# Kernel optimization log

Measured on AMD Instinct MI355X. Metric: run time of the kernel, lower is better.

The kernel has to match this reference:

```python
import jax, jax.numpy as jnp
import numpy as np

ROPE_BASE = 10000.0
NUM_HEADS = 16

def _rotate_half(x):
    d = x.shape[-1] // 2
    return jnp.concatenate([-x[..., d:], x[..., :d]], axis=-1)

def setup_inputs() -> dict:
    key = jax.random.key(0)
    ks = jax.random.split(key, 5)
    b, s, d = 1, 2048, 2048
    scale = 1.0 / np.sqrt(d)
    return {
        "hidden_states": jax.random.normal(ks[0], (b, s, d), jnp.float32),
        "wq": jax.random.normal(ks[1], (d, d), jnp.float32) * scale,
        "wk": jax.random.normal(ks[2], (d, d), jnp.float32) * scale,
        "wv": jax.random.normal(ks[3], (d, d), jnp.float32) * scale,
        "wo": jax.random.normal(ks[4], (d, d), jnp.float32) * scale,
        "position_ids": jnp.broadcast_to(jnp.arange(s, dtype=jnp.int32), (b, s)),
    }

def reference(hidden_states, wq, wk, wv, wo, position_ids):
    b, s, d = hidden_states.shape
    h = NUM_HEADS
    dh = d // h
    # q/k/v projections (torch Linear: y = x @ W^T), split heads -> bhsd
    def proj(w):
        return jnp.einsum('bsd,ed->bse', hidden_states, w).reshape(b, s, h, dh).transpose(0, 2, 1, 3)
    q, k, v = proj(wq), proj(wk), proj(wv)
    # rotary embedding (LLaMA style): freqs over half dim, duplicated
    inv_freq = 1.0 / (ROPE_BASE ** (jnp.arange(0, dh, 2, dtype=jnp.float32) / dh))
    t = jnp.arange(s, dtype=jnp.float32)
    freqs = jnp.einsum('s,f->sf', t, inv_freq)              # [s, dh/2]
    emb = jnp.concatenate([freqs, freqs], axis=-1)          # [s, dh]
    cos = jnp.cos(emb)[position_ids][:, None, :, :]         # [b,1,s,dh]
    sin = jnp.sin(emb)[position_ids][:, None, :, :]
    q = q * cos + _rotate_half(q) * sin
    k = k * cos + _rotate_half(k) * sin
    # full (non-causal) scaled dot-product attention, as in the SDPA fast path
    scores = jnp.einsum('bhqd,bhkd->bhqk', q, k) / jnp.sqrt(jnp.float32(dh))
    attn = jax.nn.softmax(scores, axis=-1)
    out = jnp.einsum('bhqk,bhkd->bhqd', attn, v)            # [b,h,s,dh]
    out = out.transpose(0, 2, 1, 3).reshape(b, s, d)
    return jnp.einsum('bsd,ed->bse', out, wo)
```

## Files before the change

kernel.cpp:

```cpp
#include <hip/hip_runtime.h>

typedef unsigned short ushort_t;
typedef unsigned int uint32;
typedef __attribute__((ext_vector_type(8))) short short8;
typedef __attribute__((ext_vector_type(4))) float f32x4;
typedef __attribute__((ext_vector_type(2))) uint32 u32x2;

#define LDS_LOAD16(gptr, lptr)                                                             \
  __builtin_amdgcn_global_load_lds((const __attribute__((address_space(1))) uint32*)(gptr),\
                                   (__attribute__((address_space(3))) uint32*)(lptr),      \
                                   16, 0, 0)

__device__ __forceinline__ ushort_t f2b(float f) {
  uint32 u = __builtin_bit_cast(uint32, f);
  u += 0x7fffu + ((u >> 16) & 1u);
  return (ushort_t)(u >> 16);
}
__device__ __forceinline__ uint32 pk2(float a, float b) {
  return (uint32)f2b(a) | ((uint32)f2b(b) << 16);
}

constexpr size_t E = (size_t)2048 * 2048;

__global__ __launch_bounds__(256) void k_cvt5(const float* __restrict__ a0, const float* __restrict__ a1,
                                              const float* __restrict__ a2, const float* __restrict__ a3,
                                              const float* __restrict__ a4, ushort_t* __restrict__ out) {
  const float* srcs[5] = {a0, a1, a2, a3, a4};
  const float* s = srcs[blockIdx.y];
  size_t i = ((size_t)blockIdx.x * 256 + threadIdx.x) * 4;
  float4 v = *(const float4*)(s + i);
  ushort4 o;
  o.x = f2b(v.x); o.y = f2b(v.y); o.z = f2b(v.z); o.w = f2b(v.w);
  *(ushort4*)(out + (size_t)blockIdx.y * E + i) = o;
}

#define SWZ3(r) (((r) >> 1) & 3)

#define STG32(srcA, srcB, dA, dB, ktile)                                        \
  do {                                                                          \
    const int koff_ = (ktile) * 32;                                             \
    _Pragma("unroll") for (int j2_ = 0; j2_ < 2; ++j2_) {                       \
      int c_ = tid + 256 * j2_;                                                 \
      int r_ = c_ >> 2, p_ = c_ & 3;                                            \
      int sc_ = (p_ ^ SWZ3(r_)) * 8;                                            \
      LDS_LOAD16((srcA) + (row0 + r_) * 2048 + koff_ + sc_, &(dA)[c_ * 8]);     \
      LDS_LOAD16((srcB) + (col0 + r_) * 2048 + koff_ + sc_, &(dB)[c_ * 8]);     \
    }                                                                           \
  } while (0)

__global__ __launch_bounds__(256, 3) void k_gemm_qkv(const ushort_t* __restrict__ A,
                                                     const ushort_t* __restrict__ B0,
                                                     const ushort_t* __restrict__ B1,
                                                     const ushort_t* __restrict__ B2,
                                                     ushort_t* __restrict__ Qm,
                                                     ushort_t* __restrict__ Km,
                                                     ushort_t* __restrict__ Vt,
                                                     const int* __restrict__ pos) {
  __shared__ ushort_t As[3][128 * 32];
  __shared__ ushort_t Bs[3][128 * 32];
  const int tid = threadIdx.x;
  const int lane = tid & 63, wave = tid >> 6;
  const int quad = lane >> 4, l16 = lane & 15;
  const int wm = wave >> 1, wn = wave & 1;
  const int z = blockIdx.z;
  const ushort_t* Bp = (z == 0) ? B0 : (z == 1) ? B1 : B2;
  const size_t row0 = (size_t)blockIdx.y * 128, col0 = (size_t)blockIdx.x * 128;

  int g[4];
#pragma unroll
  for (int j = 0; j < 4; ++j) g[j] = (j & 1) + ((j >> 1) << 2) + wn * 2;

  f32x4 zero = {0.f, 0.f, 0.f, 0.f};
  f32x4 acc[4][4];
#pragma unroll
  for (int i = 0; i < 4; ++i)
#pragma unroll
    for (int j = 0; j < 4; ++j) acc[i][j] = zero;

#define QKV_FRAGS(CUR)                                                          \
    short8 a_[4], b_[4];                                                        \
    _Pragma("unroll") for (int i_ = 0; i_ < 4; ++i_) {                          \
      int ra_ = wm * 64 + i_ * 16 + l16;                                        \
      a_[i_] = *(const short8*)&As[CUR][(ra_ * 4 + (quad ^ SWZ3(ra_))) * 8];    \
    }                                                                           \
    _Pragma("unroll") for (int j_ = 0; j_ < 4; ++j_) {                          \
      int rb_ = g[j_] * 16 + l16;                                               \
      b_[j_] = *(const short8*)&Bs[CUR][(rb_ * 4 + (quad ^ SWZ3(rb_))) * 8];    \
    }                                                                           \
    _Pragma("unroll") for (int i_ = 0; i_ < 4; ++i_)                            \
      _Pragma("unroll") for (int j_ = 0; j_ < 4; ++j_)                          \
        acc[i_][j_] = __builtin_amdgcn_mfma_f32_16x16x32_bf16(a_[i_], b_[j_], acc[i_][j_], 0, 0, 0);

#define QKV_BODY(T, CUR, STG, SEN, VM)                                          \
  do {                                                                          \
    if (SEN) STG32(A, Bp, As[STG], Bs[STG], (T) + 2);                           \
    QKV_FRAGS(CUR)                                                              \
    asm volatile("s_waitcnt " VM ::: "memory");                                 \
    __builtin_amdgcn_s_barrier();                                               \
  } while (0)

  STG32(A, Bp, As[0], Bs[0], 0);
  STG32(A, Bp, As[1], Bs[1], 1);
  asm volatile("s_waitcnt vmcnt(4)" ::: "memory");
  __builtin_amdgcn_s_barrier();

  for (int tt = 0; tt < 60; tt += 3) {
    QKV_BODY(tt + 0, 0, 2, 1, "vmcnt(4)");
    QKV_BODY(tt + 1, 1, 0, 1, "vmcnt(4)");
    QKV_BODY(tt + 2, 2, 1, 1, "vmcnt(4)");
  }
  QKV_BODY(60, 0, 2, 1, "vmcnt(4)");
  QKV_BODY(61, 1, 0, 1, "vmcnt(4)");
  QKV_BODY(62, 2, 1, 0, "vmcnt(0)");
  { QKV_FRAGS(0) }

  if (z < 2) {
    ushort_t* C = z ? Km : Qm;
    const float mul = z ? 1.0f : 0.08838834764831845f;
#pragma unroll
    for (int i = 0; i < 4; ++i)
#pragma unroll
      for (int r = 0; r < 4; ++r) {
        size_t row = row0 + wm * 64 + i * 16 + quad * 4 + r;
        float pt = (float)pos[row];
        size_t rowoff = row * 2048 + col0;
#pragma unroll
        for (int j = 0; j < 2; ++j) {
          int f = g[j] * 16 + l16;
          float ang = pt * __expf(-0.14391156831212787f * (float)f);
          float sn, cs;
          __sincosf(ang, &sn, &cs);
          cs *= mul; sn *= mul;
          float q0 = acc[i][j][r], q1 = acc[i][j + 2][r];
          C[rowoff + f]      = f2b(q0 * cs - q1 * sn);
          C[rowoff + f + 64] = f2b(q1 * cs + q0 * sn);
        }
      }
  } else {
#pragma unroll
    for (int i = 0; i < 4; ++i)
#pragma unroll
      for (int j = 0; j < 4; ++j) {
        size_t col = col0 + g[j] * 16 + l16;
        size_t rowb = row0 + wm * 64 + i * 16 + quad * 4;
        ushort4 ov;
        ov.x = f2b(acc[i][j][0]); ov.y = f2b(acc[i][j][1]);
        ov.z = f2b(acc[i][j][2]); ov.w = f2b(acc[i][j][3]);
        *(ushort4*)&Vt[col * 2048 + rowb] = ov;
      }
  }
}

__global__ __launch_bounds__(512, 2) void k_attn(const ushort_t* __restrict__ Q,
                                                 const ushort_t* __restrict__ Kg,
                                                 const ushort_t* __restrict__ Vt,
                                                 ushort_t* __restrict__ O) {
  __shared__ uint32 smem[32768];
  ushort_t* Ks0 = (ushort_t*)smem;
  ushort_t* Ks1 = (ushort_t*)(smem + 8192);
  ushort_t* Vs  = (ushort_t*)(smem + 16384);
  uint32*   Pb  = smem + 24576;
  float*    Lred = (float*)(smem + 24576);
  float*    Rbuf = (float*)smem;

  const int tid = threadIdx.x;
  const int lane = tid & 63, wave = tid >> 6;
  const int quad = lane >> 4, l16 = lane & 15;
  const int qh = wave >> 1, kh = wave & 1;
  const int bid = blockIdx.x;
  const int head = ((bid & 7) << 1) + (bid >> 7);
  const int qt = (bid >> 3) & 15;

  const ushort_t* Kbase = Kg + (size_t)head * 128;
  const ushort_t* Vbase = Vt + (size_t)head * 128 * 2048;
  uint32* Pw = Pb + wave * 1024;

  f32x4 zero = {0.f, 0.f, 0.f, 0.f};
  short8 qr[2][4];
#pragma unroll
  for (int qg = 0; qg < 2; ++qg)
#pragma unroll
    for (int kk = 0; kk < 4; ++kk)
      qr[qg][kk] = *(const short8*)&Q[(size_t)(qt * 128 + qh * 32 + qg * 16 + l16) * 2048 +
                                      head * 128 + kk * 32 + quad * 8];

  f32x4 oacc[2][8];
#pragma unroll
  for (int qg = 0; qg < 2; ++qg)
#pragma unroll
    for (int ns = 0; ns < 8; ++ns) oacc[qg][ns] = zero;
  float l_acc[2] = {0.f, 0.f};

#define STAGE_K(KD, T)                                                           \
  _Pragma("unroll") for (int j_ = 0; j_ < 4; ++j_) {                             \
    int s_ = tid + 512 * j_; int r_ = s_ >> 4, c_ = s_ & 15;                     \
    LDS_LOAD16(Kbase + (size_t)((T) * 128 + r_) * 2048 + ((c_ ^ (r_ & 15)) * 8), \
               &(KD)[s_ * 8]);                                                   \
  }
#define STAGE_V(T)                                                               \
  _Pragma("unroll") for (int j_ = 0; j_ < 4; ++j_) {                             \
    int s_ = tid + 512 * j_; int r_ = s_ >> 4, c_ = s_ & 15;                     \
    LDS_LOAD16(Vbase + (size_t)r_ * 2048 + (T) * 128 + ((c_ ^ (r_ & 15)) * 8),   \
               &Vs[s_ * 8]);                                                     \
  }

#define ATTN_BODY(KCUR, KNXT, T, NOTLAST, VMW1)                                  \
  do {                                                                           \
    STAGE_V(T);                                                                  \
    if (NOTLAST) { STAGE_K(KNXT, (T) + 1); }                                     \
    _Pragma("unroll") for (int kg = 0; kg < 4; ++kg) {                           \
      short8 kf[4];                                                              \
      _Pragma("unroll") for (int kk = 0; kk < 4; ++kk)                           \
        kf[kk] = *(const short8*)&(KCUR)[((kh * 64 + kg * 16 + l16) * 16 +       \
                                          ((kk * 4 + quad) ^ l16)) * 8];         \
      _Pragma("unroll") for (int qg = 0; qg < 2; ++qg) {                         \
        f32x4 s = zero;                                                          \
        _Pragma("unroll") for (int kk = 0; kk < 4; ++kk)                         \
          s = __builtin_amdgcn_mfma_f32_16x16x32_bf16(kf[kk], qr[qg][kk], s, 0, 0, 0); \
        float p0 = __expf(s[0]), p1 = __expf(s[1]);                              \
        float p2 = __expf(s[2]), p3 = __expf(s[3]);                              \
        l_acc[qg] += (p0 + p1) + (p2 + p3);                                      \
        u32x2 wv; wv[0] = pk2(p0, p1); wv[1] = pk2(p2, p3);                      \
        *(u32x2*)&Pw[(qg * 16 + l16) * 32 +                                      \
                     (((kg * 2 + (quad >> 1)) ^ (l16 & 7)) << 2) +               \
                     ((quad & 1) << 1)] = wv;                                    \
      }                                                                          \
    }                                                                            \
    short8 pb[2][2];                                                             \
    _Pragma("unroll") for (int qg = 0; qg < 2; ++qg)                             \
      _Pragma("unroll") for (int ks = 0; ks < 2; ++ks)                           \
        pb[qg][ks] = *(const short8*)&Pw[(qg * 16 + l16) * 32 +                  \
                                         ((((ks << 2) + quad) ^ (l16 & 7)) << 2)]; \
    asm volatile("s_waitcnt " VMW1 ::: "memory");                                \
    __builtin_amdgcn_s_barrier();                                                \
    _Pragma("unroll") for (int ns = 0; ns < 8; ++ns)                             \
      _Pragma("unroll") for (int ks = 0; ks < 2; ++ks) {                         \
        const short8 vf = *(const short8*)&Vs[((ns * 16 + l16) * 16 +            \
                                               ((kh * 8 + ks * 4 + quad) ^ l16)) * 8]; \
        _Pragma("unroll") for (int qg = 0; qg < 2; ++qg)                         \
          oacc[qg][ns] = __builtin_amdgcn_mfma_f32_16x16x32_bf16(vf, pb[qg][ks], oacc[qg][ns], 0, 0, 0); \
      }                                                                          \
    asm volatile("s_waitcnt lgkmcnt(0)" ::: "memory");                           \
    asm volatile("s_waitcnt vmcnt(0)" ::: "memory");                             \
    __builtin_amdgcn_s_barrier();                                                \
  } while (0)

  STAGE_K(Ks0, 0);
  asm volatile("s_waitcnt vmcnt(0)" ::: "memory");
  __builtin_amdgcn_s_barrier();

  for (int t2 = 0; t2 < 14; t2 += 2) {
    ATTN_BODY(Ks0, Ks1, t2 + 0, 1, "vmcnt(4)");
    ATTN_BODY(Ks1, Ks0, t2 + 1, 1, "vmcnt(4)");
  }
  ATTN_BODY(Ks0, Ks1, 14, 1, "vmcnt(4)");
  ATTN_BODY(Ks1, Ks0, 15, 0, "vmcnt(0)");

#pragma unroll
  for (int qg = 0; qg < 2; ++qg) {
    float l = l_acc[qg];
    l += __shfl_xor(l, 16, 64);
    l += __shfl_xor(l, 32, 64);
    l_acc[qg] = l;
  }
  if (quad == 0) {
#pragma unroll
    for (int qg = 0; qg < 2; ++qg) Lred[wave * 32 + qg * 16 + l16] = l_acc[qg];
  }

  const int tq = (tid >> 4) & 15;
  const int td = (tid & 15) * 8;
  for (int p = 0; p < 8; ++p) {
    __builtin_amdgcn_s_barrier();
    if ((wave >> 1) == (p >> 1)) {
      const int qg = p & 1;
#pragma unroll
      for (int ns = 0; ns < 8; ++ns)
        *(f32x4*)&Rbuf[((kh * 16 + l16)) * 132 + ns * 16 + quad * 4] = oacc[qg][ns];
    }
    __builtin_amdgcn_s_barrier();
    if (tid < 256) {
      float lt = Lred[((p >> 1) * 2 + 0) * 32 + (p & 1) * 16 + tq] +
                 Lred[((p >> 1) * 2 + 1) * 32 + (p & 1) * 16 + tq];
      float inv = 1.0f / lt;
      f32x4 sA = zero, sB = zero;
#pragma unroll
      for (int k = 0; k < 2; ++k) {
        sA += *(const f32x4*)&Rbuf[(k * 16 + tq) * 132 + td];
        sB += *(const f32x4*)&Rbuf[(k * 16 + tq) * 132 + td + 4];
      }
      ushort4 o1, o2;
      o1.x = f2b(sA[0] * inv); o1.y = f2b(sA[1] * inv);
      o1.z = f2b(sA[2] * inv); o1.w = f2b(sA[3] * inv);
      o2.x = f2b(sB[0] * inv); o2.y = f2b(sB[1] * inv);
      o2.z = f2b(sB[2] * inv); o2.w = f2b(sB[3] * inv);
      size_t orow = (size_t)(qt * 128 + (p >> 1) * 32 + (p & 1) * 16 + tq) * 2048 + head * 128 + td;
      *(ushort4*)&O[orow] = o1;
      *(ushort4*)&O[orow + 4] = o2;
    }
  }
}

__global__ __launch_bounds__(256, 3) void k_gemm_wo_sk(const ushort_t* __restrict__ A,
                                                       const ushort_t* __restrict__ B,
                                                       float* __restrict__ P) {
  __shared__ ushort_t As[3][128 * 32];
  __shared__ ushort_t Bs[3][128 * 32];
  const int tid = threadIdx.x;
  const int lane = tid & 63, wave = tid >> 6;
  const int quad = lane >> 4, l16 = lane & 15;
  const int wm = wave >> 1, wn = wave & 1;
  const size_t row0 = (size_t)blockIdx.y * 128, col0 = (size_t)blockIdx.x * 128;
  const int k0 = blockIdx.z * 1024;
  float* Pz = P + (size_t)blockIdx.z * E;
  const ushort_t* Ak = A + k0;
  const ushort_t* Bk = B + k0;

  f32x4 zero = {0.f, 0.f, 0.f, 0.f};
  f32x4 acc[4][4];
#pragma unroll
  for (int i = 0; i < 4; ++i)
#pragma unroll
    for (int j = 0; j < 4; ++j) acc[i][j] = zero;

#define WO_FRAGS(CUR)                                                           \
    short8 a_[4], b_[4];                                                        \
    _Pragma("unroll") for (int i_ = 0; i_ < 4; ++i_) {                          \
      int ra_ = wm * 64 + i_ * 16 + l16;                                        \
      a_[i_] = *(const short8*)&As[CUR][(ra_ * 4 + (quad ^ SWZ3(ra_))) * 8];    \
    }                                                                           \
    _Pragma("unroll") for (int j_ = 0; j_ < 4; ++j_) {                          \
      int rb_ = wn * 64 + j_ * 16 + l16;                                        \
      b_[j_] = *(const short8*)&Bs[CUR][(rb_ * 4 + (quad ^ SWZ3(rb_))) * 8];    \
    }                                                                           \
    _Pragma("unroll") for (int i_ = 0; i_ < 4; ++i_)                            \
      _Pragma("unroll") for (int j_ = 0; j_ < 4; ++j_)                          \
        acc[i_][j_] = __builtin_amdgcn_mfma_f32_16x16x32_bf16(a_[i_], b_[j_], acc[i_][j_], 0, 0, 0);

#define WO_BODY(T, CUR, STG, SEN, VM)                                           \
  do {                                                                          \
    if (SEN) STG32(Ak, Bk, As[STG], Bs[STG], (T) + 2);                          \
    WO_FRAGS(CUR)                                                               \
    asm volatile("s_waitcnt " VM ::: "memory");                                 \
    __builtin_amdgcn_s_barrier();                                               \
  } while (0)

  STG32(Ak, Bk, As[0], Bs[0], 0);
  STG32(Ak, Bk, As[1], Bs[1], 1);
  asm volatile("s_waitcnt vmcnt(4)" ::: "memory");
  __builtin_amdgcn_s_barrier();

  for (int tt = 0; tt < 27; tt += 3) {
    WO_BODY(tt + 0, 0, 2, 1, "vmcnt(4)");
    WO_BODY(tt + 1, 1, 0, 1, "vmcnt(4)");
    WO_BODY(tt + 2, 2, 1, 1, "vmcnt(4)");
  }
  WO_BODY(27, 0, 2, 1, "vmcnt(4)");
  WO_BODY(28, 1, 0, 1, "vmcnt(4)");
  WO_BODY(29, 2, 1, 1, "vmcnt(4)");
  WO_BODY(30, 0, 2, 0, "vmcnt(0)");
  { WO_FRAGS(1) }

#pragma unroll
  for (int i = 0; i < 4; ++i)
#pragma unroll
    for (int j = 0; j < 4; ++j)
#pragma unroll
      for (int r = 0; r < 4; ++r) {
        size_t row = row0 + wm * 64 + i * 16 + quad * 4 + r;
        size_t col = col0 + wn * 64 + j * 16 + l16;
        Pz[row * 2048 + col] = acc[i][j][r];
      }
}

__global__ __launch_bounds__(256) void k_red(const float* __restrict__ P, float* __restrict__ out) {
  size_t i = ((size_t)blockIdx.x * 256 + threadIdx.x) * 4;
  f32x4 a = *(const f32x4*)(P + i);
  f32x4 b = *(const f32x4*)(P + E + i);
  *(f32x4*)(out + i) = a + b;
}

extern "C" void kernel_launch(void* const* d_in, const int* in_sizes, int n_in,
                              void* d_out, int out_size, void* d_ws, size_t ws_size,
                              hipStream_t stream) {
  const float* X  = (const float*)d_in[0];
  const float* wq = (const float*)d_in[1];
  const float* wk = (const float*)d_in[2];
  const float* wv = (const float*)d_in[3];
  const float* wo = (const float*)d_in[4];
  const int*  pos = (const int*)d_in[5];
  float* out = (float*)d_out;

  if (ws_size < 9 * E * sizeof(ushort_t)) return;

  ushort_t* Xb  = (ushort_t*)d_ws;
  ushort_t* Wqb = Xb + E;
  ushort_t* Wkb = Xb + 2 * E;
  ushort_t* Wvb = Xb + 3 * E;
  ushort_t* Wob = Xb + 4 * E;
  ushort_t* Qm  = Xb + 5 * E;
  ushort_t* Km  = Xb + 6 * E;
  ushort_t* Vtm = Xb + 7 * E;
  ushort_t* Om  = Xb + 8 * E;
  float* Pf = (float*)Xb;

  dim3 b256(256);
  k_cvt5<<<dim3(4096, 5), b256, 0, stream>>>(X, wq, wk, wv, wo, Xb);
  k_gemm_qkv<<<dim3(16, 16, 3), b256, 0, stream>>>(Xb, Wqb, Wkb, Wvb, Qm, Km, Vtm, pos);
  k_attn<<<256, dim3(512), 0, stream>>>(Qm, Km, Vtm, Om);
  k_gemm_wo_sk<<<dim3(16, 16, 2), b256, 0, stream>>>(Om, Wob, Pf);
  k_red<<<4096, b256, 0, stream>>>(Pf, out);
}
```

Measured before the change: 266.7 us.

## Double-buffer V tiles and prefetch next K and V one iteration ahead

Adds a second LDS buffer for V, so the next K and V tiles are both issued as async global-to-LDS loads at the start of each iteration while the current tiles are consumed. Each iteration now waits only for the previous prefetch (vmcnt(8)) rather than stalling mid-iteration on V and draining all loads before the closing barrier. The goal is to hide global memory latency behind the QK and PV MFMA work. In exchange, LDS use grows from 128 KB to 160 KB per block, which leaves very little headroom for occupancy.

```diff
diff --git a/kernel.cpp b/kernel.cpp
--- a/kernel.cpp
+++ b/kernel.cpp
@@ -155,12 +155,13 @@
                                                  const ushort_t* __restrict__ Kg,
                                                  const ushort_t* __restrict__ Vt,
                                                  ushort_t* __restrict__ O) {
-  __shared__ uint32 smem[32768];
+  __shared__ uint32 smem[40960];
   ushort_t* Ks0 = (ushort_t*)smem;
   ushort_t* Ks1 = (ushort_t*)(smem + 8192);
-  ushort_t* Vs  = (ushort_t*)(smem + 16384);
-  uint32*   Pb  = smem + 24576;
-  float*    Lred = (float*)(smem + 24576);
+  ushort_t* Vs0 = (ushort_t*)(smem + 16384);
+  ushort_t* Vs1 = (ushort_t*)(smem + 24576);
+  uint32*   Pb  = smem + 32768;
+  float*    Lred = (float*)(smem + 32768);
   float*    Rbuf = (float*)smem;
 
   const int tid = threadIdx.x;
@@ -197,17 +198,19 @@
     LDS_LOAD16(Kbase + (size_t)((T) * 128 + r_) * 2048 + ((c_ ^ (r_ & 15)) * 8), \
                &(KD)[s_ * 8]);                                                   \
   }
-#define STAGE_V(T)                                                               \
+#define STAGE_V(VD, T)                                                           \
   _Pragma("unroll") for (int j_ = 0; j_ < 4; ++j_) {                             \
     int s_ = tid + 512 * j_; int r_ = s_ >> 4, c_ = s_ & 15;                     \
     LDS_LOAD16(Vbase + (size_t)r_ * 2048 + (T) * 128 + ((c_ ^ (r_ & 15)) * 8),   \
-               &Vs[s_ * 8]);                                                     \
-  }
-
-#define ATTN_BODY(KCUR, KNXT, T, NOTLAST, VMW1)                                  \
+               &(VD)[s_ * 8]);                                                   \
+  }
+
+#define ATTN_BODY(KCUR, KNXT, VCUR, VNXT, T, NOTLAST, VMW)                       \
   do {                                                                           \
-    STAGE_V(T);                                                                  \
-    if (NOTLAST) { STAGE_K(KNXT, (T) + 1); }                                     \
+    if (NOTLAST) { STAGE_K(KNXT, (T) + 1); STAGE_V(VNXT, (T) + 1); }             \
+    asm volatile("s_waitcnt " VMW ::: "memory");                                 \
+    __builtin_amdgcn_s_barrier();                                                \
+    asm volatile("" ::: "memory");                                               \
     _Pragma("unroll") for (int kg = 0; kg < 4; ++kg) {                           \
       short8 kf[4];                                                              \
       _Pragma("unroll") for (int kk = 0; kk < 4; ++kk)                           \
@@ -231,30 +234,30 @@
       _Pragma("unroll") for (int ks = 0; ks < 2; ++ks)                           \
         pb[qg][ks] = *(const short8*)&Pw[(qg * 16 + l16) * 32 +                  \
                                          ((((ks << 2) + quad) ^ (l16 & 7)) << 2)]; \
-    asm volatile("s_waitcnt " VMW1 ::: "memory");                                \
-    __builtin_amdgcn_s_barrier();                                                \
     _Pragma("unroll") for (int ns = 0; ns < 8; ++ns)                             \
       _Pragma("unroll") for (int ks = 0; ks < 2; ++ks) {                         \
-        const short8 vf = *(const short8*)&Vs[((ns * 16 + l16) * 16 +            \
+        const short8 vf = *(const short8*)&(VCUR)[((ns * 16 + l16) * 16 +        \
                                                ((kh * 8 + ks * 4 + quad) ^ l16)) * 8]; \
         _Pragma("unroll") for (int qg = 0; qg < 2; ++qg)                         \
           oacc[qg][ns] = __builtin_amdgcn_mfma_f32_16x16x32_bf16(vf, pb[qg][ks], oacc[qg][ns], 0, 0, 0); \
       }                                                                          \
-    asm volatile("s_waitcnt lgkmcnt(0)" ::: "memory");                           \
-    asm volatile("s_waitcnt vmcnt(0)" ::: "memory");                             \
+    asm volatile("" ::: "memory");                                               \
     __builtin_amdgcn_s_barrier();                                                \
+    asm volatile("" ::: "memory");                                               \
   } while (0)
 
   STAGE_K(Ks0, 0);
+  STAGE_V(Vs0, 0);
   asm volatile("s_waitcnt vmcnt(0)" ::: "memory");
   __builtin_amdgcn_s_barrier();
+  asm volatile("" ::: "memory");
 
   for (int t2 = 0; t2 < 14; t2 += 2) {
-    ATTN_BODY(Ks0, Ks1, t2 + 0, 1, "vmcnt(4)");
-    ATTN_BODY(Ks1, Ks0, t2 + 1, 1, "vmcnt(4)");
-  }
-  ATTN_BODY(Ks0, Ks1, 14, 1, "vmcnt(4)");
-  ATTN_BODY(Ks1, Ks0, 15, 0, "vmcnt(0)");
+    ATTN_BODY(Ks0, Ks1, Vs0, Vs1, t2 + 0, 1, "vmcnt(8)");
+    ATTN_BODY(Ks1, Ks0, Vs1, Vs0, t2 + 1, 1, "vmcnt(8)");
+  }
+  ATTN_BODY(Ks0, Ks1, Vs0, Vs1, 14, 1, "vmcnt(8)");
+  ATTN_BODY(Ks1, Ks0, Vs1, Vs0, 15, 0, "vmcnt(0)");
 
 #pragma unroll
   for (int qg = 0; qg < 2; ++qg) {
```

Measured after the change: 266.7 us. About the same (-0.0%).
